# Performance work log

Measured on AMD Instinct MI355X. Metric: run time of the kernel, lower is better.

## Reference

```python
import jax, jax.numpy as jnp
import numpy as np

B, C, L, H = 8, 1024, 1024, 16
DK = C // H
SCALE = 1.0 / np.sqrt(DK)


def setup_inputs() -> dict:
    key = jax.random.key(0)
    ks = jax.random.split(key, 9)
    s = 1.0 / np.sqrt(C)
    return {
        "q": jax.random.normal(ks[0], (B, C, L), dtype=jnp.float32),
        "k": jax.random.normal(ks[1], (B, C, L), dtype=jnp.float32),
        "v": jax.random.normal(ks[2], (B, C, L), dtype=jnp.float32),
        "Wq": jax.random.normal(ks[3], (C, C), dtype=jnp.float32) * s,
        "bq": jax.random.normal(ks[4], (C,), dtype=jnp.float32) * s,
        "Wk": jax.random.normal(ks[5], (C, C), dtype=jnp.float32) * s,
        "bk": jax.random.normal(ks[6], (C,), dtype=jnp.float32) * s,
        "Wv": jax.random.normal(ks[7], (C, C), dtype=jnp.float32) * s,
        "bv": jax.random.normal(ks[8], (C,), dtype=jnp.float32) * s,
    }


def _proj(x, W, b):
    # Conv1d kernel_size=1 == pointwise linear over channels: (b,c,l) -> (b,o,l)
    return jnp.einsum('oc,bcl->bol', W, x) + b[None, :, None]


def reference(q, k, v, Wq, bq, Wk, bk, Wv, bv):
    b = q.shape[0]
    qh = _proj(q, Wq, bq).reshape(b * H, DK, L)
    kh = _proj(k, Wk, bk).reshape(b * H, DK, L)
    vh = _proj(v, Wv, bv).reshape(b * H, DK, L)
    # scores[bh, t, s] = sum_c q[bh,c,t] k[bh,c,s]
    scores = jnp.einsum('bct,bcs->bts', qh, kh) * SCALE
    # NOTE: original uses nn.Softmax(dim=1) -> softmax over the query axis t
    attn = jax.nn.softmax(scores, axis=1)
    # dropout is identity in eval / p=0
    out = jnp.einsum('bts,bcs->bct', attn, vh)  # (b*H, d_k, L)
    return out.reshape(b, C, L)
```

## Files before the change

kernel.cpp:

```cpp
#include <hip/hip_runtime.h>
#include <stdint.h>

typedef unsigned short ushort_t;
typedef float  f32x4  __attribute__((ext_vector_type(4)));
typedef short  short8 __attribute__((ext_vector_type(8)));
typedef short  short4v __attribute__((ext_vector_type(4)));

#define QSCALE 0.18033688011112043f

__device__ __forceinline__ ushort_t f2bf(float f) {
  unsigned u = __builtin_bit_cast(unsigned, f);
  unsigned r = (u + 0x7fffu + ((u >> 16) & 1u)) >> 16;
  return (ushort_t)r;
}
__device__ __forceinline__ float bf2f(ushort_t u) {
  unsigned x = (unsigned)u << 16;
  return __builtin_bit_cast(float, x);
}

typedef const __attribute__((address_space(1))) unsigned int* gas_t;
typedef __attribute__((address_space(3))) unsigned int* las_t;
__device__ __forceinline__ void gload16(const void* g, void* l) {
  __builtin_amdgcn_global_load_lds((gas_t)g, (las_t)l, 16, 0, 0);
}

__global__ __launch_bounds__(256) void transpose_cvt(const float* __restrict__ in,
                                                     ushort_t* __restrict__ out) {
  __shared__ float tile[64][65];
  int b  = blockIdx.z;
  int c0 = blockIdx.x * 64, l0 = blockIdx.y * 64;
  int col = threadIdx.x & 63;
  int row4 = threadIdx.x >> 6;
  const float* p = in + ((size_t)b * 1024 + c0) * 1024 + l0;
#pragma unroll
  for (int i = 0; i < 16; ++i) {
    int r = row4 * 16 + i;
    tile[r][col] = p[(size_t)r * 1024 + col];
  }
  __syncthreads();
  ushort_t* q = out + ((size_t)b * 1024 + l0) * 1024 + c0;
#pragma unroll
  for (int i = 0; i < 16; ++i) {
    int r = row4 * 16 + i;
    q[(size_t)r * 1024 + col] = f2bf(tile[col][r]);
  }
}

__global__ __launch_bounds__(256) void cvt_bf16(const float* __restrict__ in,
                                                ushort_t* __restrict__ out, float sc) {
  int i = blockIdx.x * 256 + threadIdx.x;
  f32x4 v = *reinterpret_cast<const f32x4*>(in + (size_t)i * 4);
  short4v pk;
#pragma unroll
  for (int j = 0; j < 4; ++j) pk[j] = (short)f2bf(v[j] * sc);
  *reinterpret_cast<short4v*>(out + (size_t)i * 4) = pk;
}

template <bool OUT_T>
__global__ __launch_bounds__(256) void gemm_bt(const ushort_t* __restrict__ A,
                                               const ushort_t* __restrict__ BT,
                                               const float* __restrict__ bias,
                                               float bs,
                                               ushort_t* __restrict__ outp) {
  __shared__ ushort_t As[128 * 32];
  __shared__ ushort_t Bs[128 * 32];
  int b = blockIdx.z;
  int Mbase = blockIdx.y * 128, Nbase = blockIdx.x * 128;
  int tid = threadIdx.x;
  int lane = tid & 63, wave = tid >> 6;
  int wr = wave >> 1, wc = wave & 1;
  int lo = lane & 15, hi = lane >> 4;
  const ushort_t* Bb = BT + ((size_t)b << 20);

  f32x4 acc[4][4] = {};

  for (int kt = 0; kt < 1024; kt += 32) {
#pragma unroll
    for (int it = 0; it < 2; ++it) {
      int cch = tid + it * 256;
      int r = cch >> 2, p = cch & 3;
      gload16(A + (size_t)(Mbase + r) * 1024 + kt + p * 8, &As[it * 2048 + wave * 512]);
      gload16(Bb + (size_t)(Nbase + r) * 1024 + kt + p * 8, &Bs[it * 2048 + wave * 512]);
    }
    __syncthreads();
    short8 af[4], bf[4];
#pragma unroll
    for (int m = 0; m < 4; ++m)
      af[m] = *reinterpret_cast<const short8*>(&As[(wr * 64 + m * 16 + lo) * 32 + hi * 8]);
#pragma unroll
    for (int n = 0; n < 4; ++n)
      bf[n] = *reinterpret_cast<const short8*>(&Bs[(wc * 64 + n * 16 + lo) * 32 + hi * 8]);
#pragma unroll
    for (int m = 0; m < 4; ++m)
#pragma unroll
      for (int n = 0; n < 4; ++n)
        acc[m][n] = __builtin_amdgcn_mfma_f32_16x16x32_bf16(af[m], bf[n], acc[m][n], 0, 0, 0);
    __syncthreads();
  }

#pragma unroll
  for (int m = 0; m < 4; ++m) {
    int o0 = Mbase + wr * 64 + m * 16 + hi * 4;
#pragma unroll
    for (int n = 0; n < 4; ++n) {
      int col = Nbase + wc * 64 + n * 16 + lo;
      if (OUT_T) {
        short4v pk;
#pragma unroll
        for (int j = 0; j < 4; ++j) pk[j] = (short)f2bf(acc[m][n][j] + bias[o0 + j] * bs);
        *reinterpret_cast<short4v*>(outp + ((size_t)b << 20) + ((size_t)(o0 >> 6) << 16) +
                                    (size_t)col * 64 + (o0 & 63)) = pk;
      } else {
#pragma unroll
        for (int j = 0; j < 4; ++j)
          outp[((size_t)b << 20) + (size_t)(o0 + j) * 1024 + col] =
              f2bf(acc[m][n][j] + bias[o0 + j] * bs);
      }
    }
  }
}

__global__ __launch_bounds__(256) void attn_z(const ushort_t* __restrict__ qhT,
                                              const ushort_t* __restrict__ khT,
                                              float* __restrict__ invZ) {
  __shared__ float zbuf[2][2][64];
  int bid = blockIdx.y * 8 + blockIdx.x;
  int logical = (bid & 7) * 128 + (bid >> 3);
  int sblk = logical & 7, bh = logical >> 3;
  int tid = threadIdx.x;
  int lane = tid & 63, wave = tid >> 6;
  int wr = wave >> 1, wc = wave & 1;
  int lo = lane & 15, hi = lane >> 4;
  const ushort_t* kb = khT + ((size_t)bh << 16);
  const ushort_t* qb = qhT + ((size_t)bh << 16);

  int sbase = sblk * 128 + wr * 64;
  short8 af[4][2];
#pragma unroll
  for (int m = 0; m < 4; ++m)
#pragma unroll
    for (int kk = 0; kk < 2; ++kk)
      af[m][kk] = *reinterpret_cast<const short8*>(
          kb + (size_t)(sbase + m * 16 + lo) * 64 + kk * 32 + hi * 8);

  float zp[4][4] = {};

  for (int t0 = 0; t0 < 1024; t0 += 128) {
    int tbase = t0 + wc * 64;
    short8 bf[4][2];
#pragma unroll
    for (int n = 0; n < 4; ++n)
#pragma unroll
      for (int kk = 0; kk < 2; ++kk)
        bf[n][kk] = *reinterpret_cast<const short8*>(
            qb + (size_t)(tbase + n * 16 + lo) * 64 + kk * 32 + hi * 8);
#pragma unroll
    for (int m = 0; m < 4; ++m)
#pragma unroll
      for (int n = 0; n < 4; ++n) {
        f32x4 dd = {0.f, 0.f, 0.f, 0.f};
        dd = __builtin_amdgcn_mfma_f32_16x16x32_bf16(af[m][0], bf[n][0], dd, 0, 0, 0);
        dd = __builtin_amdgcn_mfma_f32_16x16x32_bf16(af[m][1], bf[n][1], dd, 0, 0, 0);
#pragma unroll
        for (int j = 0; j < 4; ++j) zp[m][j] += __builtin_amdgcn_exp2f(dd[j]);
      }
  }
#pragma unroll
  for (int m = 0; m < 4; ++m)
#pragma unroll
    for (int j = 0; j < 4; ++j) {
      float v = zp[m][j];
      v += __shfl_xor(v, 1);
      v += __shfl_xor(v, 2);
      v += __shfl_xor(v, 4);
      v += __shfl_xor(v, 8);
      if (lo == 0) zbuf[wc][wr][m * 16 + hi * 4 + j] = v;
    }
  __syncthreads();
  if (tid < 128) {
    float z = zbuf[0][tid >> 6][tid & 63] + zbuf[1][tid >> 6][tid & 63];
    invZ[bh * 1024 + sblk * 128 + tid] = 1.0f / z;
  }
}

__global__ __launch_bounds__(256) void vscale(ushort_t* __restrict__ vh,
                                              const float* __restrict__ invZ) {
  int bh = blockIdx.y;
  int idx = (blockIdx.x * 256 + threadIdx.x) * 8;
  int s = idx & 1023;
  ushort_t* p = vh + ((size_t)bh << 16) + idx;
  const float* iz = invZ + bh * 1024 + s;
  short8 v = *reinterpret_cast<const short8*>(p);
  short8 o;
#pragma unroll
  for (int j = 0; j < 8; ++j) o[j] = (short)f2bf(bf2f((ushort_t)v[j]) * iz[j]);
  *reinterpret_cast<short8*>(p) = o;
}

__global__ __launch_bounds__(256) void attn_av(const ushort_t* __restrict__ qhT,
                                               const ushort_t* __restrict__ khT,
                                               const ushort_t* __restrict__ vs,
                                               float* __restrict__ out) {
  __shared__ ushort_t Ks[64 * 64];
  __shared__ ushort_t Vt[64 * 64];
  __shared__ ushort_t Pt[4][32 * 64];
  int bid = blockIdx.y * 8 + blockIdx.x;
  int logical = (bid & 7) * 128 + (bid >> 3);
  int tblk = logical & 7, bh = logical >> 3;
  int tid = threadIdx.x;
  int lane = tid & 63, wave = tid >> 6;
  int lo = lane & 15, hi = lane >> 4;
  const ushort_t* qb = qhT + ((size_t)bh << 16);
  const char* kbase = (const char*)(khT + ((size_t)bh << 16));
  const char* vbase = (const char*)(vs + ((size_t)bh << 16));
  int t0 = tblk * 128 + wave * 32;

  short8 bq[2][2];
#pragma unroll
  for (int n = 0; n < 2; ++n)
#pragma unroll
    for (int kk = 0; kk < 2; ++kk)
      bq[n][kk] = *reinterpret_cast<const short8*>(
          qb + (size_t)(t0 + n * 16 + lo) * 64 + kk * 32 + hi * 8);

  f32x4 acc[4][2] = {};
  char* pw = (char*)Pt[wave];
  int swl = (lo & 7) << 4;

  for (int s0 = 0; s0 < 1024; s0 += 64) {
#pragma unroll
    for (int r = 0; r < 2; ++r) {
      int L = r * 4096 + tid * 16;
      int row = L >> 7;
      int off = (L & 127) ^ ((row & 7) << 4);
      gload16(kbase + (size_t)(s0 + row) * 128 + off,
              (char*)Ks + r * 4096 + wave * 1024);
      gload16(vbase + (size_t)row * 2048 + (size_t)s0 * 2 + off,
              (char*)Vt + r * 4096 + wave * 1024);
    }
    __syncthreads();

#pragma unroll
    for (int m = 0; m < 4; ++m) {
      int srow = m * 16 + lo;
      int sws = (srow & 7) << 4;
      short8 af0 = *reinterpret_cast<const short8*>(
          (char*)Ks + srow * 128 + ((hi * 16) ^ sws));
      short8 af1 = *reinterpret_cast<const short8*>(
          (char*)Ks + srow * 128 + ((64 + hi * 16) ^ sws));
#pragma unroll
      for (int n = 0; n < 2; ++n) {
        f32x4 dd = {0.f, 0.f, 0.f, 0.f};
        dd = __builtin_amdgcn_mfma_f32_16x16x32_bf16(af0, bq[n][0], dd, 0, 0, 0);
        dd = __builtin_amdgcn_mfma_f32_16x16x32_bf16(af1, bq[n][1], dd, 0, 0, 0);
        short4v pk;
#pragma unroll
        for (int j = 0; j < 4; ++j) pk[j] = (short)f2bf(__builtin_amdgcn_exp2f(dd[j]));
        *reinterpret_cast<short4v*>(
            pw + (n * 16 + lo) * 128 + ((m * 32 + hi * 8) ^ ((lo & 7) << 4))) = pk;
      }
    }
    asm volatile("s_waitcnt lgkmcnt(0)" ::: "memory");
    __builtin_amdgcn_sched_barrier(0);

    short8 bp[2][2];
#pragma unroll
    for (int n = 0; n < 2; ++n)
#pragma unroll
      for (int kk = 0; kk < 2; ++kk)
        bp[n][kk] = *reinterpret_cast<const short8*>(
            pw + (n * 16 + lo) * 128 + ((kk * 64 + hi * 16) ^ swl));
#pragma unroll
    for (int m = 0; m < 4; ++m) {
      int drow = m * 16 + lo;
      int swd = (drow & 7) << 4;
      short8 av0 = *reinterpret_cast<const short8*>(
          (char*)Vt + drow * 128 + ((hi * 16) ^ swd));
      short8 av1 = *reinterpret_cast<const short8*>(
          (char*)Vt + drow * 128 + ((64 + hi * 16) ^ swd));
#pragma unroll
      for (int n = 0; n < 2; ++n) {
        acc[m][n] = __builtin_amdgcn_mfma_f32_16x16x32_bf16(av0, bp[n][0], acc[m][n], 0, 0, 0);
        acc[m][n] = __builtin_amdgcn_mfma_f32_16x16x32_bf16(av1, bp[n][1], acc[m][n], 0, 0, 0);
      }
    }
    __syncthreads();
  }

  float* ob = out + ((size_t)bh << 16);
#pragma unroll
  for (int m = 0; m < 4; ++m)
#pragma unroll
    for (int n = 0; n < 2; ++n)
#pragma unroll
      for (int j = 0; j < 4; ++j)
        ob[(size_t)(m * 16 + hi * 4 + j) * 1024 + t0 + n * 16 + lo] = acc[m][n][j];
}

extern "C" void kernel_launch(void* const* d_in, const int* in_sizes, int n_in,
                              void* d_out, int out_size, void* d_ws, size_t ws_size,
                              hipStream_t stream) {
  const float* q  = (const float*)d_in[0];
  const float* k  = (const float*)d_in[1];
  const float* v  = (const float*)d_in[2];
  const float* Wq = (const float*)d_in[3];
  const float* bq = (const float*)d_in[4];
  const float* Wk = (const float*)d_in[5];
  const float* bk = (const float*)d_in[6];
  const float* Wv = (const float*)d_in[7];
  const float* bv = (const float*)d_in[8];
  float* out = (float*)d_out;
  char* ws = (char*)d_ws;
  const size_t MB = 1u << 20;

  ushort_t* xTq = (ushort_t*)(ws);
  ushort_t* xTk = (ushort_t*)(ws + 16 * MB);
  ushort_t* xTv = (ushort_t*)(ws + 32 * MB);
  ushort_t* Wqb = (ushort_t*)(ws + 48 * MB);
  ushort_t* Wkb = (ushort_t*)(ws + 50 * MB);
  ushort_t* Wvb = (ushort_t*)(ws + 52 * MB);
  ushort_t* qhT = (ushort_t*)(ws + 54 * MB);
  ushort_t* khT = xTq;
  ushort_t* vhb = xTk;
  float*    invZ = (float*)(ws + 70 * MB);

  dim3 tb(256);
  transpose_cvt<<<dim3(16, 16, 8), tb, 0, stream>>>(q, xTq);
  transpose_cvt<<<dim3(16, 16, 8), tb, 0, stream>>>(k, xTk);
  transpose_cvt<<<dim3(16, 16, 8), tb, 0, stream>>>(v, xTv);
  cvt_bf16<<<dim3(1024), tb, 0, stream>>>(Wq, Wqb, QSCALE);
  cvt_bf16<<<dim3(1024), tb, 0, stream>>>(Wk, Wkb, 1.0f);
  cvt_bf16<<<dim3(1024), tb, 0, stream>>>(Wv, Wvb, 1.0f);
  gemm_bt<true ><<<dim3(8, 8, 8), tb, 0, stream>>>(Wqb, xTq, bq, QSCALE, qhT);
  gemm_bt<true ><<<dim3(8, 8, 8), tb, 0, stream>>>(Wkb, xTk, bk, 1.0f, khT);
  gemm_bt<false><<<dim3(8, 8, 8), tb, 0, stream>>>(Wvb, xTv, bv, 1.0f, vhb);
  attn_z<<<dim3(8, 128), tb, 0, stream>>>(qhT, khT, invZ);
  vscale<<<dim3(32, 128), tb, 0, stream>>>(vhb, invZ);
  attn_av<<<dim3(8, 128), tb, 0, stream>>>(qhT, khT, vhb, out);
}
```

Measured before the change: 340.3 us.

## Batch prep launches, fuse V scaling into Z kernel, double-buffer attn_av K/V

Merges the three input transposes and three weight conversions into one launch each, removing per-launch overhead. The V column scaling by 1/Z is folded into the Z-sum kernel, so the invZ round trip through global memory and the separate vscale launch go away. attn_av now double-buffers the K/V tiles in LDS and prefetches the next tile while computing the current one, replacing per-iteration full syncs with vmcnt waits and barriers. s_setprio hints are added around MFMA sections. The extra LDS buffers may lower occupancy.

```diff
diff --git a/kernel.cpp b/kernel.cpp
--- a/kernel.cpp
+++ b/kernel.cpp
@@ -24,10 +24,15 @@
   __builtin_amdgcn_global_load_lds((gas_t)g, (las_t)l, 16, 0, 0);
 }
 
-__global__ __launch_bounds__(256) void transpose_cvt(const float* __restrict__ in,
-                                                     ushort_t* __restrict__ out) {
+__global__ __launch_bounds__(256) void transpose_cvt3(
+    const float* __restrict__ q, const float* __restrict__ k,
+    const float* __restrict__ v, ushort_t* __restrict__ oq,
+    ushort_t* __restrict__ ok, ushort_t* __restrict__ ov) {
   __shared__ float tile[64][65];
-  int b  = blockIdx.z;
+  int z = blockIdx.z;
+  int t = z >> 3, b = z & 7;
+  const float* in = (t == 0) ? q : (t == 1) ? k : v;
+  ushort_t* out = (t == 0) ? oq : (t == 1) ? ok : ov;
   int c0 = blockIdx.x * 64, l0 = blockIdx.y * 64;
   int col = threadIdx.x & 63;
   int row4 = threadIdx.x >> 6;
@@ -38,17 +43,23 @@
     tile[r][col] = p[(size_t)r * 1024 + col];
   }
   __syncthreads();
-  ushort_t* q = out + ((size_t)b * 1024 + l0) * 1024 + c0;
+  ushort_t* qo = out + ((size_t)b * 1024 + l0) * 1024 + c0;
 #pragma unroll
   for (int i = 0; i < 16; ++i) {
     int r = row4 * 16 + i;
-    q[(size_t)r * 1024 + col] = f2bf(tile[col][r]);
-  }
-}
-
-__global__ __launch_bounds__(256) void cvt_bf16(const float* __restrict__ in,
-                                                ushort_t* __restrict__ out, float sc) {
-  int i = blockIdx.x * 256 + threadIdx.x;
+    qo[(size_t)r * 1024 + col] = f2bf(tile[col][r]);
+  }
+}
+
+__global__ __launch_bounds__(256) void cvt_w3(
+    const float* __restrict__ Wq, const float* __restrict__ Wk,
+    const float* __restrict__ Wv, ushort_t* __restrict__ oq,
+    ushort_t* __restrict__ ok, ushort_t* __restrict__ ov) {
+  int seg = blockIdx.x >> 10;
+  const float* in = (seg == 0) ? Wq : (seg == 1) ? Wk : Wv;
+  ushort_t* out = (seg == 0) ? oq : (seg == 1) ? ok : ov;
+  float sc = (seg == 0) ? QSCALE : 1.0f;
+  int i = (blockIdx.x & 1023) * 256 + threadIdx.x;
   f32x4 v = *reinterpret_cast<const f32x4*>(in + (size_t)i * 4);
   short4v pk;
 #pragma unroll
@@ -120,10 +131,11 @@
   }
 }
 
-__global__ __launch_bounds__(256) void attn_z(const ushort_t* __restrict__ qhT,
-                                              const ushort_t* __restrict__ khT,
-                                              float* __restrict__ invZ) {
+__global__ __launch_bounds__(256) void attn_zs(const ushort_t* __restrict__ qhT,
+                                               const ushort_t* __restrict__ khT,
+                                               ushort_t* __restrict__ vhb) {
   __shared__ float zbuf[2][2][64];
+  __shared__ float invs[128];
   int bid = blockIdx.y * 8 + blockIdx.x;
   int logical = (bid & 7) * 128 + (bid >> 3);
   int sblk = logical & 7, bh = logical >> 3;
@@ -159,8 +171,10 @@
 #pragma unroll
       for (int n = 0; n < 4; ++n) {
         f32x4 dd = {0.f, 0.f, 0.f, 0.f};
+        __builtin_amdgcn_s_setprio(1);
         dd = __builtin_amdgcn_mfma_f32_16x16x32_bf16(af[m][0], bf[n][0], dd, 0, 0, 0);
         dd = __builtin_amdgcn_mfma_f32_16x16x32_bf16(af[m][1], bf[n][1], dd, 0, 0, 0);
+        __builtin_amdgcn_s_setprio(0);
 #pragma unroll
         for (int j = 0; j < 4; ++j) zp[m][j] += __builtin_amdgcn_exp2f(dd[j]);
       }
@@ -177,32 +191,29 @@
       if (lo == 0) zbuf[wc][wr][m * 16 + hi * 4 + j] = v;
     }
   __syncthreads();
-  if (tid < 128) {
-    float z = zbuf[0][tid >> 6][tid & 63] + zbuf[1][tid >> 6][tid & 63];
-    invZ[bh * 1024 + sblk * 128 + tid] = 1.0f / z;
-  }
-}
-
-__global__ __launch_bounds__(256) void vscale(ushort_t* __restrict__ vh,
-                                              const float* __restrict__ invZ) {
-  int bh = blockIdx.y;
-  int idx = (blockIdx.x * 256 + threadIdx.x) * 8;
-  int s = idx & 1023;
-  ushort_t* p = vh + ((size_t)bh << 16) + idx;
-  const float* iz = invZ + bh * 1024 + s;
-  short8 v = *reinterpret_cast<const short8*>(p);
-  short8 o;
-#pragma unroll
-  for (int j = 0; j < 8; ++j) o[j] = (short)f2bf(bf2f((ushort_t)v[j]) * iz[j]);
-  *reinterpret_cast<short8*>(p) = o;
+  if (tid < 128)
+    invs[tid] = 1.0f / (zbuf[0][tid >> 6][tid & 63] + zbuf[1][tid >> 6][tid & 63]);
+  __syncthreads();
+
+  int d = tid >> 2, soff = (tid & 3) * 32;
+  ushort_t* vp = vhb + ((size_t)bh << 16) + (size_t)d * 1024 + sblk * 128 + soff;
+#pragma unroll
+  for (int c = 0; c < 4; ++c) {
+    short8 vv = *reinterpret_cast<const short8*>(vp + c * 8);
+    short8 o;
+#pragma unroll
+    for (int j = 0; j < 8; ++j)
+      o[j] = (short)f2bf(bf2f((ushort_t)vv[j]) * invs[soff + c * 8 + j]);
+    *reinterpret_cast<short8*>(vp + c * 8) = o;
+  }
 }
 
 __global__ __launch_bounds__(256) void attn_av(const ushort_t* __restrict__ qhT,
                                                const ushort_t* __restrict__ khT,
                                                const ushort_t* __restrict__ vs,
                                                float* __restrict__ out) {
-  __shared__ ushort_t Ks[64 * 64];
-  __shared__ ushort_t Vt[64 * 64];
+  __shared__ ushort_t Ks[2][64 * 64];
+  __shared__ ushort_t Vt[2][64 * 64];
   __shared__ ushort_t Pt[4][32 * 64];
   int bid = blockIdx.y * 8 + blockIdx.x;
   int logical = (bid & 7) * 128 + (bid >> 3);
@@ -227,37 +238,40 @@
   char* pw = (char*)Pt[wave];
   int swl = (lo & 7) << 4;
 
-  for (int s0 = 0; s0 < 1024; s0 += 64) {
+  auto stageKV = [&](int buf, int s0) {
 #pragma unroll
     for (int r = 0; r < 2; ++r) {
       int L = r * 4096 + tid * 16;
       int row = L >> 7;
       int off = (L & 127) ^ ((row & 7) << 4);
       gload16(kbase + (size_t)(s0 + row) * 128 + off,
-              (char*)Ks + r * 4096 + wave * 1024);
+              (char*)Ks + buf * 8192 + r * 4096 + wave * 1024);
       gload16(vbase + (size_t)row * 2048 + (size_t)s0 * 2 + off,
-              (char*)Vt + r * 4096 + wave * 1024);
-    }
-    __syncthreads();
-
+              (char*)Vt + buf * 8192 + r * 4096 + wave * 1024);
+    }
+  };
+
+  auto computeTile = [&](int buf) {
+    char* ksb = (char*)Ks + buf * 8192;
+    char* vtb = (char*)Vt + buf * 8192;
 #pragma unroll
     for (int m = 0; m < 4; ++m) {
       int srow = m * 16 + lo;
       int sws = (srow & 7) << 4;
-      short8 af0 = *reinterpret_cast<const short8*>(
-          (char*)Ks + srow * 128 + ((hi * 16) ^ sws));
-      short8 af1 = *reinterpret_cast<const short8*>(
-          (char*)Ks + srow * 128 + ((64 + hi * 16) ^ sws));
+      short8 af0 = *reinterpret_cast<const short8*>(ksb + srow * 128 + ((hi * 16) ^ sws));
+      short8 af1 = *reinterpret_cast<const short8*>(ksb + srow * 128 + ((64 + hi * 16) ^ sws));
 #pragma unroll
       for (int n = 0; n < 2; ++n) {
         f32x4 dd = {0.f, 0.f, 0.f, 0.f};
+        __builtin_amdgcn_s_setprio(1);
         dd = __builtin_amdgcn_mfma_f32_16x16x32_bf16(af0, bq[n][0], dd, 0, 0, 0);
         dd = __builtin_amdgcn_mfma_f32_16x16x32_bf16(af1, bq[n][1], dd, 0, 0, 0);
+        __builtin_amdgcn_s_setprio(0);
         short4v pk;
 #pragma unroll
         for (int j = 0; j < 4; ++j) pk[j] = (short)f2bf(__builtin_amdgcn_exp2f(dd[j]));
         *reinterpret_cast<short4v*>(
-            pw + (n * 16 + lo) * 128 + ((m * 32 + hi * 8) ^ ((lo & 7) << 4))) = pk;
+            pw + (n * 16 + lo) * 128 + ((m * 32 + hi * 8) ^ swl)) = pk;
       }
     }
     asm volatile("s_waitcnt lgkmcnt(0)" ::: "memory");
@@ -270,22 +284,36 @@
       for (int kk = 0; kk < 2; ++kk)
         bp[n][kk] = *reinterpret_cast<const short8*>(
             pw + (n * 16 + lo) * 128 + ((kk * 64 + hi * 16) ^ swl));
+    __builtin_amdgcn_s_setprio(1);
 #pragma unroll
     for (int m = 0; m < 4; ++m) {
       int drow = m * 16 + lo;
       int swd = (drow & 7) << 4;
-      short8 av0 = *reinterpret_cast<const short8*>(
-          (char*)Vt + drow * 128 + ((hi * 16) ^ swd));
-      short8 av1 = *reinterpret_cast<const short8*>(
-          (char*)Vt + drow * 128 + ((64 + hi * 16) ^ swd));
+      short8 av0 = *reinterpret_cast<const short8*>(vtb + drow * 128 + ((hi * 16) ^ swd));
+      short8 av1 = *reinterpret_cast<const short8*>(vtb + drow * 128 + ((64 + hi * 16) ^ swd));
 #pragma unroll
       for (int n = 0; n < 2; ++n) {
         acc[m][n] = __builtin_amdgcn_mfma_f32_16x16x32_bf16(av0, bp[n][0], acc[m][n], 0, 0, 0);
         acc[m][n] = __builtin_amdgcn_mfma_f32_16x16x32_bf16(av1, bp[n][1], acc[m][n], 0, 0, 0);
       }
     }
-    __syncthreads();
-  }
+    __builtin_amdgcn_s_setprio(0);
+  };
+
+  stageKV(0, 0);
+#pragma unroll 1
+  for (int i = 0; i < 15; ++i) {
+    stageKV((i + 1) & 1, (i + 1) * 64);
+    asm volatile("s_waitcnt vmcnt(4)" ::: "memory");
+    __builtin_amdgcn_s_barrier();
+    __builtin_amdgcn_sched_barrier(0);
+    computeTile(i & 1);
+    __builtin_amdgcn_s_barrier();
+  }
+  asm volatile("s_waitcnt vmcnt(0)" ::: "memory");
+  __builtin_amdgcn_s_barrier();
+  __builtin_amdgcn_sched_barrier(0);
+  computeTile(1);
 
   float* ob = out + ((size_t)bh << 16);
 #pragma unroll
@@ -322,19 +350,13 @@
   ushort_t* qhT = (ushort_t*)(ws + 54 * MB);
   ushort_t* khT = xTq;
   ushort_t* vhb = xTk;
-  float*    invZ = (float*)(ws + 70 * MB);
 
   dim3 tb(256);
-  transpose_cvt<<<dim3(16, 16, 8), tb, 0, stream>>>(q, xTq);
-  transpose_cvt<<<dim3(16, 16, 8), tb, 0, stream>>>(k, xTk);
-  transpose_cvt<<<dim3(16, 16, 8), tb, 0, stream>>>(v, xTv);
-  cvt_bf16<<<dim3(1024), tb, 0, stream>>>(Wq, Wqb, QSCALE);
-  cvt_bf16<<<dim3(1024), tb, 0, stream>>>(Wk, Wkb, 1.0f);
-  cvt_bf16<<<dim3(1024), tb, 0, stream>>>(Wv, Wvb, 1.0f);
+  transpose_cvt3<<<dim3(16, 16, 24), tb, 0, stream>>>(q, k, v, xTq, xTk, xTv);
+  cvt_w3<<<dim3(3072), tb, 0, stream>>>(Wq, Wk, Wv, Wqb, Wkb, Wvb);
   gemm_bt<true ><<<dim3(8, 8, 8), tb, 0, stream>>>(Wqb, xTq, bq, QSCALE, qhT);
   gemm_bt<true ><<<dim3(8, 8, 8), tb, 0, stream>>>(Wkb, xTk, bk, 1.0f, khT);
   gemm_bt<false><<<dim3(8, 8, 8), tb, 0, stream>>>(Wvb, xTv, bv, 1.0f, vhb);
-  attn_z<<<dim3(8, 128), tb, 0, stream>>>(qhT, khT, invZ);
-  vscale<<<dim3(32, 128), tb, 0, stream>>>(vhb, invZ);
+  attn_zs<<<dim3(8, 128), tb, 0, stream>>>(qhT, khT, vhb);
   attn_av<<<dim3(8, 128), tb, 0, stream>>>(qhT, khT, vhb, out);
 }
```

Result: faster. 333.6 us (-2.0%).
